# Kernel optimization log

Hardware: AMD Instinct MI355X
Metric: run time of the kernel (lower is better)

Reference implementation:

```python
import jax, jax.numpy as jnp
import numpy as np

N_NODES = 100000
N_EDGES = 3200000
HID = 32
N_LAYERS = 3
MAX_Z = 1000
K = 30
N_GRAPHS = 2000
NPG = N_NODES // N_GRAPHS          # 50 nodes per graph (equal-size graphs)
TLD = HID * N_LAYERS + 1           # total_latent_dim = 97
DENSE = ((K - 2) // 2 + 1 - 5 + 1) * 32  # 352


def _init(key, shape, fan_in):
    return jax.random.normal(key, shape, jnp.float32) / np.sqrt(fan_in)


def setup_inputs():
    key = jax.random.key(0)
    ks = jax.random.split(key, 24)
    z = jax.random.randint(ks[0], (N_NODES,), 0, MAX_Z)
    edge_index = jax.random.randint(ks[1], (2, N_EDGES), 0, N_NODES)
    batch = jnp.repeat(jnp.arange(N_GRAPHS), NPG)  # sorted, equal-size graphs
    inp = {"z": z, "edge_index": edge_index, "batch": batch}
    inp["z_table"] = _init(ks[2], (MAX_Z, HID), HID)
    # GCN stack: (in->h), (h->h), (h->h), (h->1)
    dims = [(HID, HID), (HID, HID), (HID, HID), (HID, 1)]
    for i, (di, do) in enumerate(dims):
        inp[f"W{i}"] = _init(ks[3 + 2 * i], (di, do), di)
        inp[f"b{i}"] = jnp.zeros((do,), jnp.float32)
    inp["conv1_w"] = _init(ks[12], (16, 1, TLD), TLD)
    inp["conv1_b"] = jnp.zeros((16,), jnp.float32)
    inp["conv2_w"] = _init(ks[13], (32, 16, 5), 16 * 5)
    inp["conv2_b"] = jnp.zeros((32,), jnp.float32)
    inp["lin1_w"] = _init(ks[14], (DENSE, 128), DENSE)
    inp["lin1_b"] = jnp.zeros((128,), jnp.float32)
    inp["lin2_w"] = _init(ks[15], (128, 1), 128)
    inp["lin2_b"] = jnp.zeros((1,), jnp.float32)
    return inp


def gcn_conv(x, src, dst, W, b):
    # PyG GCNConv: h = x @ W, then symmetric-normalized propagation with self-loops, + bias.
    h = x @ W
    deg = jnp.zeros((N_NODES,), h.dtype).at[dst].add(1.0) + 1.0  # +1 self loop
    dinv = jax.lax.rsqrt(deg)
    coef = dinv[src] * dinv[dst]                                  # [E]
    out = jnp.zeros_like(h).at[dst].add(h[src] * coef[:, None])   # neighbor agg
    out = out + h * (dinv * dinv)[:, None]                        # self-loop term
    return out + b


def conv1d(x, w, b, stride):
    y = jax.lax.conv_general_dilated(x, w, (stride,), 'VALID',
                                     dimension_numbers=('NCH', 'OIH', 'NCH'))
    return y + b[None, :, None]


def sort_pool(x, k):
    # global_sort_pool with equal-size graphs: sort nodes within each graph by
    # last feature channel (descending), keep top-k, flatten.
    xb = x.reshape(N_GRAPHS, NPG, -1)
    order = jnp.argsort(-xb[:, :, -1], axis=1)[:, :k]             # [B, k]
    xk = jnp.take_along_axis(xb, order[:, :, None], axis=1)       # [B, k, D]
    return xk.reshape(N_GRAPHS, -1)


def reference(z, edge_index, batch, z_table, W0, b0, W1, b1, W2, b2, W3, b3,
              conv1_w, conv1_b, conv2_w, conv2_b, lin1_w, lin1_b, lin2_w, lin2_b):
    src, dst = edge_index[0], edge_index[1]
    h = z_table[z]                                   # [N, HID]
    xs = []
    for W, b in ((W0, b0), (W1, b1), (W2, b2), (W3, b3)):
        h = jnp.tanh(gcn_conv(h, src, dst, W, b))
        xs.append(h)
    x = jnp.concatenate(xs, axis=-1)                 # [N, 97]
    x = sort_pool(x, K)[:, None, :]                  # [B, 1, K*97]
    x = jax.nn.relu(conv1d(x, conv1_w, conv1_b, TLD))  # [B, 16, K]
    B, C, L = x.shape
    x = x.reshape(B, C, L // 2, 2).max(-1)           # maxpool1d(2,2) -> [B,16,15]
    x = jax.nn.relu(conv1d(x, conv2_w, conv2_b, 1))  # [B, 32, 11]
    x = x.reshape(B, -1)                             # [B, 352]
    x = jax.nn.relu(x @ lin1_w + lin1_b)             # dropout is identity at eval
    return x @ lin2_w + lin2_b                       # [B, 1]
```

## Files before the change

kernel.cpp:

```cpp
#include <hip/hip_runtime.h>
#include <hip/hip_bf16.h>
#include <math.h>

#define N_NODES 100000
#define N_EDGES 3200000
#define HID 32
#define K_TOP 30
#define N_GRAPHS 2000
#define NPG 50
#define TLD 97
#define DENSE 352

#define NB 256
#define NPB 391
#define CAP 14336
#define NBLK 512
#define CE  ((N_EDGES + NBLK - 1) / NBLK)

__global__ __launch_bounds__(256) void k_bucket(const int* __restrict__ dst,
                                                const int* __restrict__ src,
                                                int* __restrict__ gcount,
                                                int* __restrict__ buf) {
    __shared__ int hist[NB];
    __shared__ int base_l[NB];
    int tid = threadIdx.x;
    int e0 = blockIdx.x * CE;
    int e1 = e0 + CE; if (e1 > N_EDGES) e1 = N_EDGES;
    hist[tid] = 0;
    __syncthreads();
    for (int e = e0 + tid; e < e1; e += 256) {
        int d = dst[e];
        atomicAdd(&hist[d / NPB], 1);
    }
    __syncthreads();
    int cnt = hist[tid];
    base_l[tid] = cnt ? atomicAdd(&gcount[tid], cnt) : 0;
    __syncthreads();
    hist[tid] = 0;
    __syncthreads();
    for (int e = e0 + tid; e < e1; e += 256) {
        int d = dst[e];
        int s = src[e];
        int b = d / NPB;
        int r = atomicAdd(&hist[b], 1);
        buf[b * CAP + base_l[b] + r] = ((d - b * NPB) << 17) | s;
    }
}

__global__ __launch_bounds__(512) void k_build(const int* __restrict__ buf,
                                               const int* __restrict__ gcount,
                                               int* __restrict__ row_ptr,
                                               float* __restrict__ dinv,
                                               int* __restrict__ col) {
    __shared__ int sb[NB];
    __shared__ int s[512];
    int k = blockIdx.x;
    int tid = threadIdx.x;
    if (tid < NB) sb[tid] = gcount[tid];
    __syncthreads();
    for (int off = 1; off < NB; off <<= 1) {
        int t = (tid < NB && tid >= off) ? sb[tid - off] : 0;
        __syncthreads();
        if (tid < NB) sb[tid] += t;
        __syncthreads();
    }
    int rowbase = (k == 0) ? 0 : sb[k - 1];
    int cnt = gcount[k];
    if (k == NB - 1 && tid == 0) row_ptr[N_NODES] = sb[NB - 1];
    int lo = k * NPB;
    const int* b = buf + k * CAP;
    s[tid] = 0;
    __syncthreads();
    for (int i = tid; i < cnt; i += 512)
        atomicAdd(&s[b[i] >> 17], 1);
    __syncthreads();
    int mydeg = s[tid];
    bool valid = (tid < NPB) && (lo + tid < N_NODES);
    if (valid) dinv[lo + tid] = rsqrtf((float)(mydeg + 1));
    for (int off = 1; off < 512; off <<= 1) {
        int t = (tid >= off) ? s[tid - off] : 0;
        __syncthreads();
        s[tid] += t;
        __syncthreads();
    }
    int excl = s[tid] - mydeg;
    if (valid) row_ptr[lo + tid] = rowbase + excl;
    __syncthreads();
    s[tid] = excl;
    __syncthreads();
    for (int i = tid; i < cnt; i += 512) {
        int v = b[i];
        int r = atomicAdd(&s[v >> 17], 1);
        col[rowbase + r] = v & 0x1FFFF;
    }
}

__global__ void k_embed_lin0(const int* __restrict__ z, const float* __restrict__ zt,
                             const float* __restrict__ W, const float* __restrict__ dinv,
                             float* __restrict__ hs) {
    __shared__ float Ws[32 * 32];
    int tid = threadIdx.x;
    for (int i = tid; i < 1024; i += 256) Ws[i] = W[i];
    __syncthreads();
    int gi = blockIdx.x * 256 + tid;
    if (gi >= N_NODES * 32) return;
    int n = gi >> 5, f = gi & 31;
    float v = zt[z[n] * 32 + f];
    float acc = 0.f;
#pragma unroll
    for (int f2 = 0; f2 < 32; ++f2)
        acc += __shfl(v, f2, 32) * Ws[f2 * 32 + f];
    hs[gi] = acc * dinv[n];
}

__device__ __forceinline__ float gather32(const float* __restrict__ hs,
                                          const int* __restrict__ col,
                                          int beg, int end, int f, float acc) {
    for (int base = beg; base < end; base += 32) {
        int rem = end - base;
        int m = rem >= 32 ? 32 : rem;
        int c = (f < m) ? col[base + f] : 0;
        float vals[32];
#pragma unroll
        for (int i = 0; i < 32; ++i) {
            int ci = __shfl(c, i, 32);
            vals[i] = hs[ci * 32 + f];
        }
        if (m == 32) {
#pragma unroll
            for (int i = 0; i < 32; ++i) acc += vals[i];
        } else {
#pragma unroll
            for (int i = 0; i < 32; ++i)
                if (i < m) acc += vals[i];
        }
    }
    return acc;
}

__global__ void k_layer(const float* __restrict__ hs, const int* __restrict__ row_ptr,
                        const int* __restrict__ col, const float* __restrict__ dinv,
                        const float* __restrict__ b, const float* __restrict__ Wnext,
                        float* __restrict__ xcat, int coloff,
                        float* __restrict__ hs_out) {
    __shared__ float Ws[32 * 32];
    int tid = threadIdx.x;
    for (int i = tid; i < 1024; i += 256) Ws[i] = Wnext[i];
    __syncthreads();
    int gi = blockIdx.x * 256 + tid;
    if (gi >= N_NODES * 32) return;
    int n = gi >> 5, f = gi & 31;
    int beg = row_ptr[n], end = row_ptr[n + 1];
    float acc = hs[n * 32 + f];
    acc = gather32(hs, col, beg, end, f, acc);
    float v = tanhf(acc * dinv[n] + b[f]);
    xcat[n * 97 + coloff + f] = v;
    float a2 = 0.f;
#pragma unroll
    for (int f2 = 0; f2 < 32; ++f2)
        a2 += __shfl(v, f2, 32) * Ws[f2 * 32 + f];
    hs_out[n * 32 + f] = a2 * dinv[n];
}

__global__ void k_layer_last(const float* __restrict__ hs, const int* __restrict__ row_ptr,
                             const int* __restrict__ col, const float* __restrict__ dinv,
                             const float* __restrict__ b, const float* __restrict__ W3,
                             float* __restrict__ xcat, int coloff,
                             float* __restrict__ h4) {
    int gi = blockIdx.x * 256 + threadIdx.x;
    if (gi >= N_NODES * 32) return;
    int n = gi >> 5, f = gi & 31;
    int beg = row_ptr[n], end = row_ptr[n + 1];
    float acc = hs[n * 32 + f];
    acc = gather32(hs, col, beg, end, f, acc);
    float v = tanhf(acc * dinv[n] + b[f]);
    xcat[n * 97 + coloff + f] = v;
    float p = v * W3[f];
#pragma unroll
    for (int off = 16; off >= 1; off >>= 1) p += __shfl_xor(p, off);
    if (f == 0) h4[n] = p * dinv[n];
}

__global__ void k_prop1w(const float* __restrict__ hs4, const int* __restrict__ row_ptr,
                         const int* __restrict__ col, const float* __restrict__ dinv,
                         const float* __restrict__ b3, float* __restrict__ xcat) {
    int gi = blockIdx.x * 256 + threadIdx.x;
    if (gi >= N_NODES * 32) return;
    int n = gi >> 5, lane = gi & 31;
    int beg = row_ptr[n], end = row_ptr[n + 1];
    float part = 0.f;
    for (int e = beg + lane; e < end; e += 32)
        part += hs4[col[e]];
#pragma unroll
    for (int off = 16; off >= 1; off >>= 1) part += __shfl_xor(part, off);
    if (lane == 0) {
        float acc = hs4[n] + part;
        xcat[n * 97 + 96] = tanhf(acc * dinv[n] + b3[0]);
    }
}

__global__ __launch_bounds__(128) void k_head(
    const float* __restrict__ xcat,
    const float* __restrict__ w1, const float* __restrict__ b1,
    const float* __restrict__ w2, const float* __restrict__ b2,
    const float* __restrict__ l1w, const float* __restrict__ l1b,
    const float* __restrict__ l2w, const float* __restrict__ l2b,
    float* __restrict__ out) {
    __shared__ float xk[K_TOP][97];
    __shared__ float w1s[16 * 97];
    __shared__ float w2s[32 * 80];
    __shared__ float y1[16][K_TOP];
    __shared__ float y1p[16][15];
    __shared__ float y2[DENSE];
    __shared__ float z1[128];
    __shared__ int   sel[K_TOP];
    __shared__ float red[2];

    int g = blockIdx.x;
    int tid = threadIdx.x;
    int base = g * NPG;

    for (int i = tid; i < 16 * 97; i += 128) w1s[i] = w1[i];
    for (int i = tid; i < 32 * 80; i += 128) w2s[i] = w2[i];

    if (tid < 64) {
        float v; int idx;
        if (tid < NPG) { v = xcat[(base + tid) * 97 + 96]; idx = tid; }
        else           { v = -INFINITY;                    idx = 64 + tid; }
        for (int k = 2; k <= 64; k <<= 1) {
            for (int j = k >> 1; j > 0; j >>= 1) {
                float ov = __shfl_xor(v, j);
                int   oi = __shfl_xor(idx, j);
                bool lower = (tid & j) == 0;
                bool dirA  = (tid & k) == 0;
                bool mineFirst = (v > ov) || (v == ov && idx < oi);
                bool keep = lower ? (mineFirst == dirA) : (mineFirst != dirA);
                if (!keep) { v = ov; idx = oi; }
            }
        }
        if (tid < K_TOP) sel[tid] = idx;
    }
    __syncthreads();

    for (int i = tid; i < K_TOP * 97; i += 128) {
        int j = i / 97, d = i - j * 97;
        xk[j][d] = xcat[(base + sel[j]) * 97 + d];
    }
    __syncthreads();

    for (int i = tid; i < 16 * K_TOP; i += 128) {
        int c = i / K_TOP, j = i - c * K_TOP;
        float acc = b1[c];
#pragma unroll
        for (int d = 0; d < 97; ++d) acc += xk[j][d] * w1s[c * 97 + d];
        y1[c][j] = fmaxf(acc, 0.f);
    }
    __syncthreads();

    for (int i = tid; i < 16 * 15; i += 128) {
        int c = i / 15, p = i - c * 15;
        y1p[c][p] = fmaxf(y1[c][2 * p], y1[c][2 * p + 1]);
    }
    __syncthreads();

    for (int i = tid; i < 32 * 11; i += 128) {
        int o = i / 11, p = i - o * 11;
        float acc = b2[o];
#pragma unroll
        for (int ci = 0; ci < 16; ++ci)
#pragma unroll
            for (int t = 0; t < 5; ++t)
                acc += y1p[ci][p + t] * w2s[o * 80 + ci * 5 + t];
        y2[o * 11 + p] = fmaxf(acc, 0.f);
    }
    __syncthreads();

    {
        float acc = l1b[tid];
        for (int r = 0; r < DENSE; ++r) acc += y2[r] * l1w[r * 128 + tid];
        z1[tid] = fmaxf(acc, 0.f);
    }
    __syncthreads();

    float p = z1[tid] * l2w[tid];
    for (int off = 32; off >= 1; off >>= 1) p += __shfl_xor(p, off);
    if ((tid & 63) == 0) red[tid >> 6] = p;
    __syncthreads();
    if (tid == 0) out[g] = red[0] + red[1] + l2b[0];
}

extern "C" void kernel_launch(void* const* d_in, const int* in_sizes, int n_in,
                              void* d_out, int out_size, void* d_ws, size_t ws_size,
                              hipStream_t stream) {
    const int*   z   = (const int*)d_in[0];
    const int*   ei  = (const int*)d_in[1];
    const float* zt  = (const float*)d_in[3];
    const float* W0  = (const float*)d_in[4];  const float* b0  = (const float*)d_in[5];
    const float* W1  = (const float*)d_in[6];  const float* b1g = (const float*)d_in[7];
    const float* W2  = (const float*)d_in[8];  const float* b2g = (const float*)d_in[9];
    const float* W3  = (const float*)d_in[10]; const float* b3  = (const float*)d_in[11];
    const float* c1w = (const float*)d_in[12]; const float* c1b = (const float*)d_in[13];
    const float* c2w = (const float*)d_in[14]; const float* c2b = (const float*)d_in[15];
    const float* l1w = (const float*)d_in[16]; const float* l1b = (const float*)d_in[17];
    const float* l2w = (const float*)d_in[18]; const float* l2b = (const float*)d_in[19];
    float* out = (float*)d_out;

    char* ws = (char*)d_ws;
    size_t off = 0;
    auto alloc = [&](size_t bytes) {
        void* p = ws + off;
        off += (bytes + 255) & ~(size_t)255;
        return p;
    };
    int*   row_ptr   = (int*)alloc((size_t)(N_NODES + 1) * 4);
    float* dinv      = (float*)alloc((size_t)N_NODES * 4);
    int*   col       = (int*)alloc((size_t)N_EDGES * 4);
    int*   gcount    = (int*)alloc((size_t)NB * 4);
    int*   bucketbuf = (int*)alloc((size_t)NB * CAP * 4);
    float* hA        = (float*)alloc((size_t)N_NODES * 32 * 4);
    float* hB        = (float*)alloc((size_t)N_NODES * 32 * 4);
    float* h4        = (float*)alloc((size_t)N_NODES * 4);
    float* xcat      = (float*)alloc((size_t)N_NODES * 97 * 4);

    const int* srcp = ei;
    const int* dstp = ei + N_EDGES;

    hipMemsetAsync(gcount, 0, (size_t)NB * 4, stream);

    int nf = (N_NODES * 32 + 255) / 256;

    k_bucket<<<NBLK, 256, 0, stream>>>(dstp, srcp, gcount, bucketbuf);
    k_build<<<NB, 512, 0, stream>>>(bucketbuf, gcount, row_ptr, dinv, col);

    k_embed_lin0<<<nf, 256, 0, stream>>>(z, zt, W0, dinv, hA);
    k_layer<<<nf, 256, 0, stream>>>(hA, row_ptr, col, dinv, b0, W1, xcat, 0, hB);
    k_layer<<<nf, 256, 0, stream>>>(hB, row_ptr, col, dinv, b1g, W2, xcat, 32, hA);
    k_layer_last<<<nf, 256, 0, stream>>>(hA, row_ptr, col, dinv, b2g, W3, xcat, 64, h4);
    k_prop1w<<<nf, 256, 0, stream>>>(h4, row_ptr, col, dinv, b3, xcat);

    k_head<<<N_GRAPHS, 128, 0, stream>>>(xcat, c1w, c1b, c2w, c2b,
                                         l1w, l1b, l2w, l2b, out);
}
```

Before: 455.8 us.

## Gather neighbor features with float4 loads, 8 lanes per node

The GCN layer kernels switch from 32 lanes per node with scalar feature loads to 8 lanes per node, each lane loading and accumulating a float4 of features. Neighbor indices are now broadcast within 8-lane groups, and the dense 32x32 transform reads float4 weights from shared memory. This cuts load instruction count and lets each wave cover four times as many nodes, which should help the gather-bound layers. In exchange, the smaller chunks of 8 edges give less memory-level parallelism per node, and the xcat writes stay scalar.

```diff
diff --git a/kernel.cpp b/kernel.cpp
--- a/kernel.cpp
+++ b/kernel.cpp
@@ -113,72 +113,117 @@
     hs[gi] = acc * dinv[n];
 }
 
-__device__ __forceinline__ float gather32(const float* __restrict__ hs,
-                                          const int* __restrict__ col,
-                                          int beg, int end, int f, float acc) {
-    for (int base = beg; base < end; base += 32) {
-        int rem = end - base;
-        int m = rem >= 32 ? 32 : rem;
-        int c = (f < m) ? col[base + f] : 0;
-        float vals[32];
-#pragma unroll
-        for (int i = 0; i < 32; ++i) {
-            int ci = __shfl(c, i, 32);
-            vals[i] = hs[ci * 32 + f];
+__device__ __forceinline__ void gather8(const float* __restrict__ hs,
+                                        const int* __restrict__ col,
+                                        int beg, int end, int j, float4& acc) {
+    int deg = end - beg;
+    int nch = (deg + 7) >> 3;
+    for (int it = 0; it < nch; ++it) {
+        int eidx = beg + (it << 3) + j;
+        int cj = (eidx < end) ? col[eidx] : 0;
+        float4 vals[8];
+#pragma unroll
+        for (int i = 0; i < 8; ++i) {
+            int ci = __shfl(cj, i, 8);
+            vals[i] = *(const float4*)&hs[ci * 32 + 4 * j];
         }
-        if (m == 32) {
-#pragma unroll
-            for (int i = 0; i < 32; ++i) acc += vals[i];
+        int rem = deg - (it << 3);
+        if (rem >= 8) {
+#pragma unroll
+            for (int i = 0; i < 8; ++i) {
+                acc.x += vals[i].x; acc.y += vals[i].y;
+                acc.z += vals[i].z; acc.w += vals[i].w;
+            }
         } else {
 #pragma unroll
-            for (int i = 0; i < 32; ++i)
-                if (i < m) acc += vals[i];
+            for (int i = 0; i < 8; ++i)
+                if (i < rem) {
+                    acc.x += vals[i].x; acc.y += vals[i].y;
+                    acc.z += vals[i].z; acc.w += vals[i].w;
+                }
         }
     }
-    return acc;
-}
-
-__global__ void k_layer(const float* __restrict__ hs, const int* __restrict__ row_ptr,
+}
+
+__global__ __launch_bounds__(256) void k_layer(const float* __restrict__ hs,
+                        const int* __restrict__ row_ptr,
                         const int* __restrict__ col, const float* __restrict__ dinv,
                         const float* __restrict__ b, const float* __restrict__ Wnext,
                         float* __restrict__ xcat, int coloff,
                         float* __restrict__ hs_out) {
-    __shared__ float Ws[32 * 32];
-    int tid = threadIdx.x;
-    for (int i = tid; i < 1024; i += 256) Ws[i] = Wnext[i];
-    __syncthreads();
-    int gi = blockIdx.x * 256 + tid;
-    if (gi >= N_NODES * 32) return;
-    int n = gi >> 5, f = gi & 31;
+    __shared__ float4 Ws[32][8];
+    int tid = threadIdx.x;
+    {
+        int f = tid >> 3, j = tid & 7;
+        Ws[f][j] = make_float4(Wnext[f * 32 + 4 * j], Wnext[f * 32 + 4 * j + 1],
+                               Wnext[f * 32 + 4 * j + 2], Wnext[f * 32 + 4 * j + 3]);
+    }
+    __syncthreads();
+    int n = blockIdx.x * 32 + (tid >> 3);
+    int j = tid & 7;
+    float dn = dinv[n];
     int beg = row_ptr[n], end = row_ptr[n + 1];
-    float acc = hs[n * 32 + f];
-    acc = gather32(hs, col, beg, end, f, acc);
-    float v = tanhf(acc * dinv[n] + b[f]);
-    xcat[n * 97 + coloff + f] = v;
-    float a2 = 0.f;
-#pragma unroll
-    for (int f2 = 0; f2 < 32; ++f2)
-        a2 += __shfl(v, f2, 32) * Ws[f2 * 32 + f];
-    hs_out[n * 32 + f] = a2 * dinv[n];
-}
-
-__global__ void k_layer_last(const float* __restrict__ hs, const int* __restrict__ row_ptr,
+    float4 acc = *(const float4*)&hs[n * 32 + 4 * j];
+    gather8(hs, col, beg, end, j, acc);
+    float4 vv;
+    vv.x = tanhf(acc.x * dn + b[4 * j + 0]);
+    vv.y = tanhf(acc.y * dn + b[4 * j + 1]);
+    vv.z = tanhf(acc.z * dn + b[4 * j + 2]);
+    vv.w = tanhf(acc.w * dn + b[4 * j + 3]);
+    xcat[n * 97 + coloff + 4 * j + 0] = vv.x;
+    xcat[n * 97 + coloff + 4 * j + 1] = vv.y;
+    xcat[n * 97 + coloff + 4 * j + 2] = vv.z;
+    xcat[n * 97 + coloff + 4 * j + 3] = vv.w;
+    float4 o = make_float4(0.f, 0.f, 0.f, 0.f);
+#pragma unroll
+    for (int jj = 0; jj < 8; ++jj) {
+        float vx = __shfl(vv.x, jj, 8);
+        float vy = __shfl(vv.y, jj, 8);
+        float vz = __shfl(vv.z, jj, 8);
+        float vw = __shfl(vv.w, jj, 8);
+        float4 w0 = Ws[4 * jj + 0][j];
+        float4 w1 = Ws[4 * jj + 1][j];
+        float4 w2 = Ws[4 * jj + 2][j];
+        float4 w3 = Ws[4 * jj + 3][j];
+        o.x += vx * w0.x; o.x += vy * w1.x; o.x += vz * w2.x; o.x += vw * w3.x;
+        o.y += vx * w0.y; o.y += vy * w1.y; o.y += vz * w2.y; o.y += vw * w3.y;
+        o.z += vx * w0.z; o.z += vy * w1.z; o.z += vz * w2.z; o.z += vw * w3.z;
+        o.w += vx * w0.w; o.w += vy * w1.w; o.w += vz * w2.w; o.w += vw * w3.w;
+    }
+    *(float4*)&hs_out[n * 32 + 4 * j] =
+        make_float4(o.x * dn, o.y * dn, o.z * dn, o.w * dn);
+}
+
+__global__ __launch_bounds__(256) void k_layer_last(const float* __restrict__ hs,
+                             const int* __restrict__ row_ptr,
                              const int* __restrict__ col, const float* __restrict__ dinv,
                              const float* __restrict__ b, const float* __restrict__ W3,
                              float* __restrict__ xcat, int coloff,
                              float* __restrict__ h4) {
-    int gi = blockIdx.x * 256 + threadIdx.x;
-    if (gi >= N_NODES * 32) return;
-    int n = gi >> 5, f = gi & 31;
+    int tid = threadIdx.x;
+    int n = blockIdx.x * 32 + (tid >> 3);
+    int j = tid & 7;
+    float dn = dinv[n];
     int beg = row_ptr[n], end = row_ptr[n + 1];
-    float acc = hs[n * 32 + f];
-    acc = gather32(hs, col, beg, end, f, acc);
-    float v = tanhf(acc * dinv[n] + b[f]);
-    xcat[n * 97 + coloff + f] = v;
-    float p = v * W3[f];
-#pragma unroll
-    for (int off = 16; off >= 1; off >>= 1) p += __shfl_xor(p, off);
-    if (f == 0) h4[n] = p * dinv[n];
+    float4 acc = *(const float4*)&hs[n * 32 + 4 * j];
+    gather8(hs, col, beg, end, j, acc);
+    float4 vv;
+    vv.x = tanhf(acc.x * dn + b[4 * j + 0]);
+    vv.y = tanhf(acc.y * dn + b[4 * j + 1]);
+    vv.z = tanhf(acc.z * dn + b[4 * j + 2]);
+    vv.w = tanhf(acc.w * dn + b[4 * j + 3]);
+    xcat[n * 97 + coloff + 4 * j + 0] = vv.x;
+    xcat[n * 97 + coloff + 4 * j + 1] = vv.y;
+    xcat[n * 97 + coloff + 4 * j + 2] = vv.z;
+    xcat[n * 97 + coloff + 4 * j + 3] = vv.w;
+    float p = vv.x * W3[4 * j + 0];
+    p += vv.y * W3[4 * j + 1];
+    p += vv.z * W3[4 * j + 2];
+    p += vv.w * W3[4 * j + 3];
+    p += __shfl_xor(p, 1, 8);
+    p += __shfl_xor(p, 2, 8);
+    p += __shfl_xor(p, 4, 8);
+    if (j == 0) h4[n] = p * dn;
 }
 
 __global__ void k_prop1w(const float* __restrict__ hs4, const int* __restrict__ row_ptr,
@@ -328,14 +373,15 @@
     hipMemsetAsync(gcount, 0, (size_t)NB * 4, stream);
 
     int nf = (N_NODES * 32 + 255) / 256;
+    int nl = N_NODES / 32;
 
     k_bucket<<<NBLK, 256, 0, stream>>>(dstp, srcp, gcount, bucketbuf);
     k_build<<<NB, 512, 0, stream>>>(bucketbuf, gcount, row_ptr, dinv, col);
 
     k_embed_lin0<<<nf, 256, 0, stream>>>(z, zt, W0, dinv, hA);
-    k_layer<<<nf, 256, 0, stream>>>(hA, row_ptr, col, dinv, b0, W1, xcat, 0, hB);
-    k_layer<<<nf, 256, 0, stream>>>(hB, row_ptr, col, dinv, b1g, W2, xcat, 32, hA);
-    k_layer_last<<<nf, 256, 0, stream>>>(hA, row_ptr, col, dinv, b2g, W3, xcat, 64, h4);
+    k_layer<<<nl, 256, 0, stream>>>(hA, row_ptr, col, dinv, b0, W1, xcat, 0, hB);
+    k_layer<<<nl, 256, 0, stream>>>(hB, row_ptr, col, dinv, b1g, W2, xcat, 32, hA);
+    k_layer_last<<<nl, 256, 0, stream>>>(hA, row_ptr, col, dinv, b2g, W3, xcat, 64, h4);
     k_prop1w<<<nf, 256, 0, stream>>>(h4, row_ptr, col, dinv, b3, xcat);
 
     k_head<<<N_GRAPHS, 128, 0, stream>>>(xcat, c1w, c1b, c2w, c2b,
```

After: 444.4 us. -2.5%, faster.
